# Kernel optimization log

Hardware: AMD Instinct MI355X
Metric: run time of the kernel (lower is better)

## Reference

```python
import jax, jax.numpy as jnp
import numpy as np

F = 256          # number of features (input_size)
H1, H2, H3 = 128, 64, 32
OUT = 1          # output_size


def setup_inputs() -> dict:
    key = jax.random.key(0)
    ks = jax.random.split(key, 10)
    B = 8192
    # Kaiming-uniform-ish small init; exact init doesn't matter for a math reference.
    def w(k, shape, fan_in):
        lim = 1.0 / np.sqrt(fan_in)
        return jax.random.uniform(k, shape, jnp.float32, -lim, lim)
    return {
        "x": jax.random.normal(ks[0], (B, F), dtype=jnp.float32),
        "W1": w(ks[1], (F, H1), 1),          # Linear(1 -> H1) per feature
        "b1": w(ks[2], (F, H1), 1),
        "W2": w(ks[3], (F, H1, H2), H1),
        "b2": w(ks[4], (F, H2), H1),
        "W3": w(ks[5], (F, H2, H3), H2),
        "b3": w(ks[6], (F, H3), H2),
        "W4": w(ks[7], (F, H3, OUT), H3),
        "b4": w(ks[8], (F, OUT), H3),
        "bias": jnp.zeros((OUT,), dtype=jnp.float32),
    }


def reference(x, W1, b1, W2, b2, W3, b3, W4, b4, bias):
    # Fused form of the per-feature FeatureNN loop (eval mode: dropout = identity).
    # Layer 1: scalar input per feature -> H1
    h = jax.nn.relu(x[:, :, None] * W1[None, :, :] + b1[None, :, :])   # [B,F,H1]
    h = jax.nn.relu(jnp.einsum('bfh,fhk->bfk', h, W2) + b2[None])      # [B,F,H2]
    h = jax.nn.relu(jnp.einsum('bfh,fhk->bfk', h, W3) + b3[None])      # [B,F,H3]
    f_out = jnp.einsum('bfh,fhk->bfk', h, W4) + b4[None]               # [B,F,OUT]
    # torch.cat(dim=1).sum(dim=1, keepdim=True): sum over features and output cols
    out = jnp.sum(f_out, axis=(1, 2), keepdims=False)[:, None] + bias[None, :]
    return out  # [B, OUT] with OUT==1
```

## Files before the change

kernel.cpp:

```cpp
#include <hip/hip_runtime.h>
#include <math.h>


#define NF   256
#define NH1  128
#define NH2  64
#define NH3  32
#define NB   8192

#define NRANK 129
#define ROW4  17
#define ROWH  136

typedef float    f32x4 __attribute__((ext_vector_type(4)));
typedef unsigned u32x4 __attribute__((ext_vector_type(4)));
typedef _Float16 h16x2 __attribute__((ext_vector_type(2)));
typedef _Float16 h16x8 __attribute__((ext_vector_type(8)));

__device__ __forceinline__ unsigned pkh2(unsigned sw, unsigned sb, h16x2 xh) {
    h16x2 r = __builtin_elementwise_fma(xh, __builtin_bit_cast(h16x2, sw),
                                            __builtin_bit_cast(h16x2, sb));
    h16x2 hz = {(_Float16)0.f, (_Float16)0.f};
    return __builtin_bit_cast(unsigned, __builtin_elementwise_max(r, hz));
}

__global__ __launch_bounds__(256) void init_out_kernel(float* __restrict__ out,
                                                       const float* __restrict__ bias) {
    int i = blockIdx.x * 256 + threadIdx.x;
    if (i < NB) out[i] = bias[0];
}

__global__ __launch_bounds__(1024, 8) void nam_fused(
    const float* __restrict__ x,
    const float* __restrict__ W1, const float* __restrict__ b1,
    const float* __restrict__ W2, const float* __restrict__ b2,
    const float* __restrict__ W3, const float* __restrict__ b3,
    const float* __restrict__ W4, const float* __restrict__ b4,
    float* __restrict__ out)
{
    __shared__ u32x4 SP4[NRANK * ROW4];
    __shared__ float tkey[NH1];
    __shared__ int   tidx[NH1];
    __shared__ float w1s[NH1], b1s[NH1];
    __shared__ float Pbw[8][NH2], Pbb[8][NH2], Pdw[8][NH2], Pdb[8][NH2];

    const int f    = blockIdx.x >> 1;
    const int half = blockIdx.x & 1;
    const int t = (int)threadIdx.x;
    _Float16* SPh = (_Float16*)SP4;

    const float* __restrict__ gw2 = W2 + (size_t)f * NH1 * NH2;
    if (t < NH1) {
        float w  = W1[f * NH1 + t];
        float bb = b1[f * NH1 + t];
        w1s[t] = w; b1s[t] = bb;
        tkey[t] = (w != 0.0f) ? (-bb / w) : INFINITY;
        tidx[t] = t;
    }
    __syncthreads();

    for (int size = 2; size <= NH1; size <<= 1) {
        for (int stride = size >> 1; stride > 0; stride >>= 1) {
            if (t < 64) {
                int pos = ((t / stride) * (stride << 1)) + (t % stride);
                int par = pos + stride;
                bool up = ((pos & size) == 0);
                float a = tkey[pos], c = tkey[par];
                int  ia = tidx[pos], ic = tidx[par];
                if ((a > c) == up) {
                    tkey[pos] = c; tkey[par] = a;
                    tidx[pos] = ic; tidx[par] = ia;
                }
            }
            __syncthreads();
        }
    }

    if (t < 512) {
        const int k = t & 63, c = t >> 6;
        float bw = 0.0f, bbp = 0.0f, dw = 0.0f, db = 0.0f;
        #pragma unroll 4
        for (int i = 0; i < 16; ++i) {
            int j = c * 16 + i;
            float w = w1s[j], bv = b1s[j], w2v = gw2[j * NH2 + k];
            if (w < 0.0f) { bw = fmaf(w, w2v, bw); bbp = fmaf(bv, w2v, bbp); }
            else if (w == 0.0f && bv > 0.0f) { bbp = fmaf(bv, w2v, bbp); }
            int jj = tidx[c * 16 + i];
            float ww = w1s[jj], bv2 = b1s[jj], w2x = gw2[jj * NH2 + k];
            float s = (ww > 0.0f) ? 1.0f : ((ww < 0.0f) ? -1.0f : 0.0f);
            dw = fmaf(s * ww,  w2x, dw);
            db = fmaf(s * bv2, w2x, db);
        }
        Pbw[c][k] = bw; Pbb[c][k] = bbp; Pdw[c][k] = dw; Pdb[c][k] = db;
    }
    __syncthreads();
    if (t < 512) {
        const int k = t & 63, c = t >> 6;
        float accw = 0.0f;
        float accb = b2[f * NH2 + k];
        #pragma unroll
        for (int c2 = 0; c2 < 8; ++c2) { accw += Pbw[c2][k]; accb += Pbb[c2][k]; }
        for (int c2 = 0; c2 < c; ++c2) { accw += Pdw[c2][k]; accb += Pdb[c2][k]; }
        if (c == 0) {
            SPh[k]      = (_Float16)accw;
            SPh[64 + k] = (_Float16)accb;
        }
        #pragma unroll 4
        for (int i = 0; i < 16; ++i) {
            int r = c * 16 + i;
            int j = tidx[r];
            float w = w1s[j], bv = b1s[j], w2v = gw2[j * NH2 + k];
            float s = (w > 0.0f) ? 1.0f : ((w < 0.0f) ? -1.0f : 0.0f);
            accw = fmaf(s * w,  w2v, accw);
            accb = fmaf(s * bv, w2v, accb);
            SPh[(r + 1) * ROWH + k]      = (_Float16)accw;
            SPh[(r + 1) * ROWH + 64 + k] = (_Float16)accb;
        }
    }
    __syncthreads();

    const int lane = t & 63, wv = t >> 6;
    const int n = lane & 15, q = lane >> 4;

    const float* __restrict__ w3g = W3 + f * NH2 * NH3;
    h16x8 aT0lo, aT0hi, aT1lo, aT1hi;
    #pragma unroll
    for (int j = 0; j < 8; ++j) {
        int k = q * 8 + j;
        aT0lo[j] = (_Float16)w3g[k * NH3 + n];
        aT0hi[j] = (_Float16)w3g[(k + 32) * NH3 + n];
        aT1lo[j] = (_Float16)w3g[k * NH3 + n + 16];
        aT1hi[j] = (_Float16)w3g[(k + 32) * NH3 + n + 16];
    }
    float b3c[4], b3ch[4], w4c[4], w4ch[4];
    #pragma unroll
    for (int i = 0; i < 4; ++i) {
        b3c[i]  = b3[f * NH3 + q * 4 + i];
        b3ch[i] = b3[f * NH3 + 16 + q * 4 + i];
        w4c[i]  = W4[f * NH3 + q * 4 + i];
        w4ch[i] = W4[f * NH3 + 16 + q * 4 + i];
    }
    const float b4f = b4[f];

    #pragma unroll 1
    for (int round = 0; round < 16; ++round) {
        const int base = half * 4096 + (round * 16 + wv) * 16;
        const int b = base + n;
        const float xv = x[(size_t)b * NF + f];

        int r = 0;
        #pragma unroll
        for (int s = 64; s > 0; s >>= 1)
            if (tkey[r + s - 1] < xv) r += s;

        const int ro = r * ROW4;
        u32x4 SW0 = SP4[ro + q],     SW1 = SP4[ro + 4 + q];
        u32x4 SB0 = SP4[ro + 8 + q], SB1 = SP4[ro + 12 + q];

        const h16x2 xh = {(_Float16)xv, (_Float16)xv};
        u32x4 d0, d1;
        d0.x = pkh2(SW0.x, SB0.x, xh);
        d0.y = pkh2(SW0.y, SB0.y, xh);
        d0.z = pkh2(SW0.z, SB0.z, xh);
        d0.w = pkh2(SW0.w, SB0.w, xh);
        d1.x = pkh2(SW1.x, SB1.x, xh);
        d1.y = pkh2(SW1.y, SB1.y, xh);
        d1.z = pkh2(SW1.z, SB1.z, xh);
        d1.w = pkh2(SW1.w, SB1.w, xh);
        h16x8 bf0 = __builtin_bit_cast(h16x8, d0);
        h16x8 bf1 = __builtin_bit_cast(h16x8, d1);

        f32x4 acc0 = {b3c[0], b3c[1], b3c[2], b3c[3]};
        f32x4 acc1 = {b3ch[0], b3ch[1], b3ch[2], b3ch[3]};
        acc0 = __builtin_amdgcn_mfma_f32_16x16x32_f16(aT0lo, bf0, acc0, 0, 0, 0);
        acc0 = __builtin_amdgcn_mfma_f32_16x16x32_f16(aT0hi, bf1, acc0, 0, 0, 0);
        acc1 = __builtin_amdgcn_mfma_f32_16x16x32_f16(aT1lo, bf0, acc1, 0, 0, 0);
        acc1 = __builtin_amdgcn_mfma_f32_16x16x32_f16(aT1hi, bf1, acc1, 0, 0, 0);

        float p = fmaxf(acc0[0], 0.0f) * w4c[0] + fmaxf(acc1[0], 0.0f) * w4ch[0]
                + fmaxf(acc0[1], 0.0f) * w4c[1] + fmaxf(acc1[1], 0.0f) * w4ch[1]
                + fmaxf(acc0[2], 0.0f) * w4c[2] + fmaxf(acc1[2], 0.0f) * w4ch[2]
                + fmaxf(acc0[3], 0.0f) * w4c[3] + fmaxf(acc1[3], 0.0f) * w4ch[3];
        p += __shfl_xor(p, 16);
        p += __shfl_xor(p, 32);
        if (lane < 16) atomicAdd(&out[base + lane], p + b4f);
    }
}

extern "C" void kernel_launch(void* const* d_in, const int* in_sizes, int n_in,
                              void* d_out, int out_size, void* d_ws, size_t ws_size,
                              hipStream_t stream) {
    const float* x    = (const float*)d_in[0];
    const float* W1   = (const float*)d_in[1];
    const float* b1   = (const float*)d_in[2];
    const float* W2   = (const float*)d_in[3];
    const float* b2   = (const float*)d_in[4];
    const float* W3   = (const float*)d_in[5];
    const float* b3   = (const float*)d_in[6];
    const float* W4   = (const float*)d_in[7];
    const float* b4   = (const float*)d_in[8];
    const float* bias = (const float*)d_in[9];
    float* out = (float*)d_out;

    init_out_kernel<<<NB / 256, 256, 0, stream>>>(out, bias);
    nam_fused<<<NF * 2, 1024, 0, stream>>>(x, W1, b1, W2, b2,
                                           W3, b3, W4, b4, out);
}
```

Before: 126.4 us.

## Switch layer-3 MFMA to 32x32x16 tiles and hoist top binary-search levels to registers

Each wave now processes 32 batch rows per round with four 32x32x16 f16 MFMAs instead of 16 rows with four 16x16x32 MFMAs, halving the number of rounds, per-row shuffle reductions and atomic-issue rounds. The first three levels of the breakpoint binary search are resolved from tkey values cached in registers, which removes three shared-memory loads per lookup. In exchange each thread holds more accumulator and weight registers, which may pressure occupancy under the 1024x8 launch bounds.

```diff
diff --git a/kernel.cpp b/kernel.cpp
--- a/kernel.cpp
+++ b/kernel.cpp
@@ -12,10 +12,10 @@
 #define ROW4  17
 #define ROWH  136
 
-typedef float    f32x4 __attribute__((ext_vector_type(4)));
-typedef unsigned u32x4 __attribute__((ext_vector_type(4)));
-typedef _Float16 h16x2 __attribute__((ext_vector_type(2)));
-typedef _Float16 h16x8 __attribute__((ext_vector_type(8)));
+typedef float    f32x16 __attribute__((ext_vector_type(16)));
+typedef unsigned u32x4  __attribute__((ext_vector_type(4)));
+typedef _Float16 h16x2  __attribute__((ext_vector_type(2)));
+typedef _Float16 h16x8  __attribute__((ext_vector_type(8)));
 
 __device__ __forceinline__ unsigned pkh2(unsigned sw, unsigned sb, h16x2 xh) {
     h16x2 r = __builtin_elementwise_fma(xh, __builtin_bit_cast(h16x2, sw),
@@ -120,70 +120,82 @@
     __syncthreads();
 
     const int lane = t & 63, wv = t >> 6;
-    const int n = lane & 15, q = lane >> 4;
+    const int n = lane & 31, q2 = lane >> 5;
 
     const float* __restrict__ w3g = W3 + f * NH2 * NH3;
-    h16x8 aT0lo, aT0hi, aT1lo, aT1hi;
+    h16x8 A0, A1, A2, A3;
     #pragma unroll
     for (int j = 0; j < 8; ++j) {
-        int k = q * 8 + j;
-        aT0lo[j] = (_Float16)w3g[k * NH3 + n];
-        aT0hi[j] = (_Float16)w3g[(k + 32) * NH3 + n];
-        aT1lo[j] = (_Float16)w3g[k * NH3 + n + 16];
-        aT1hi[j] = (_Float16)w3g[(k + 32) * NH3 + n + 16];
-    }
-    float b3c[4], b3ch[4], w4c[4], w4ch[4];
+        int kk = q2 * 8 + j;
+        A0[j] = (_Float16)w3g[kk * NH3 + n];
+        A1[j] = (_Float16)w3g[(kk + 16) * NH3 + n];
+        A2[j] = (_Float16)w3g[(kk + 32) * NH3 + n];
+        A3[j] = (_Float16)w3g[(kk + 48) * NH3 + n];
+    }
+    float b3r[16], w4r[16];
     #pragma unroll
-    for (int i = 0; i < 4; ++i) {
-        b3c[i]  = b3[f * NH3 + q * 4 + i];
-        b3ch[i] = b3[f * NH3 + 16 + q * 4 + i];
-        w4c[i]  = W4[f * NH3 + q * 4 + i];
-        w4ch[i] = W4[f * NH3 + 16 + q * 4 + i];
+    for (int reg = 0; reg < 16; ++reg) {
+        int row = (reg & 3) + 8 * (reg >> 2) + 4 * q2;
+        b3r[reg] = b3[f * NH3 + row];
+        w4r[reg] = W4[f * NH3 + row];
     }
     const float b4f = b4[f];
+    const float t63 = tkey[63], t31 = tkey[31], t95 = tkey[95];
+    const float t15 = tkey[15], t47 = tkey[47], t79 = tkey[79], t111 = tkey[111];
 
     #pragma unroll 1
-    for (int round = 0; round < 16; ++round) {
-        const int base = half * 4096 + (round * 16 + wv) * 16;
-        const int b = base + n;
-        const float xv = x[(size_t)b * NF + f];
-
-        int r = 0;
-        #pragma unroll
-        for (int s = 64; s > 0; s >>= 1)
+    for (int round = 0; round < 8; ++round) {
+        const int base = half * 4096 + (round * 16 + wv) * 32;
+        const float xv = x[(size_t)(base + n) * NF + f];
+
+        int r = (t63 < xv) ? 64 : 0;
+        {
+            float l1 = (r & 64) ? t95 : t31;
+            if (l1 < xv) r += 32;
+            float m0 = (r & 64) ? t79  : t15;
+            float m1 = (r & 64) ? t111 : t47;
+            float l2 = (r & 32) ? m1 : m0;
+            if (l2 < xv) r += 16;
+        }
+        #pragma unroll
+        for (int s = 8; s > 0; s >>= 1)
             if (tkey[r + s - 1] < xv) r += s;
 
         const int ro = r * ROW4;
-        u32x4 SW0 = SP4[ro + q],     SW1 = SP4[ro + 4 + q];
-        u32x4 SB0 = SP4[ro + 8 + q], SB1 = SP4[ro + 12 + q];
+        u32x4 SW0 = SP4[ro + q2],      SW1 = SP4[ro + 2 + q2];
+        u32x4 SW2 = SP4[ro + 4 + q2],  SW3 = SP4[ro + 6 + q2];
+        u32x4 SB0 = SP4[ro + 8 + q2],  SB1 = SP4[ro + 10 + q2];
+        u32x4 SB2 = SP4[ro + 12 + q2], SB3 = SP4[ro + 14 + q2];
 
         const h16x2 xh = {(_Float16)xv, (_Float16)xv};
-        u32x4 d0, d1;
-        d0.x = pkh2(SW0.x, SB0.x, xh);
-        d0.y = pkh2(SW0.y, SB0.y, xh);
-        d0.z = pkh2(SW0.z, SB0.z, xh);
-        d0.w = pkh2(SW0.w, SB0.w, xh);
-        d1.x = pkh2(SW1.x, SB1.x, xh);
-        d1.y = pkh2(SW1.y, SB1.y, xh);
-        d1.z = pkh2(SW1.z, SB1.z, xh);
-        d1.w = pkh2(SW1.w, SB1.w, xh);
-        h16x8 bf0 = __builtin_bit_cast(h16x8, d0);
-        h16x8 bf1 = __builtin_bit_cast(h16x8, d1);
-
-        f32x4 acc0 = {b3c[0], b3c[1], b3c[2], b3c[3]};
-        f32x4 acc1 = {b3ch[0], b3ch[1], b3ch[2], b3ch[3]};
-        acc0 = __builtin_amdgcn_mfma_f32_16x16x32_f16(aT0lo, bf0, acc0, 0, 0, 0);
-        acc0 = __builtin_amdgcn_mfma_f32_16x16x32_f16(aT0hi, bf1, acc0, 0, 0, 0);
-        acc1 = __builtin_amdgcn_mfma_f32_16x16x32_f16(aT1lo, bf0, acc1, 0, 0, 0);
-        acc1 = __builtin_amdgcn_mfma_f32_16x16x32_f16(aT1hi, bf1, acc1, 0, 0, 0);
-
-        float p = fmaxf(acc0[0], 0.0f) * w4c[0] + fmaxf(acc1[0], 0.0f) * w4ch[0]
-                + fmaxf(acc0[1], 0.0f) * w4c[1] + fmaxf(acc1[1], 0.0f) * w4ch[1]
-                + fmaxf(acc0[2], 0.0f) * w4c[2] + fmaxf(acc1[2], 0.0f) * w4ch[2]
-                + fmaxf(acc0[3], 0.0f) * w4c[3] + fmaxf(acc1[3], 0.0f) * w4ch[3];
-        p += __shfl_xor(p, 16);
+        u32x4 d0, d1, d2, d3;
+        d0.x = pkh2(SW0.x, SB0.x, xh); d0.y = pkh2(SW0.y, SB0.y, xh);
+        d0.z = pkh2(SW0.z, SB0.z, xh); d0.w = pkh2(SW0.w, SB0.w, xh);
+        d1.x = pkh2(SW1.x, SB1.x, xh); d1.y = pkh2(SW1.y, SB1.y, xh);
+        d1.z = pkh2(SW1.z, SB1.z, xh); d1.w = pkh2(SW1.w, SB1.w, xh);
+        d2.x = pkh2(SW2.x, SB2.x, xh); d2.y = pkh2(SW2.y, SB2.y, xh);
+        d2.z = pkh2(SW2.z, SB2.z, xh); d2.w = pkh2(SW2.w, SB2.w, xh);
+        d3.x = pkh2(SW3.x, SB3.x, xh); d3.y = pkh2(SW3.y, SB3.y, xh);
+        d3.z = pkh2(SW3.z, SB3.z, xh); d3.w = pkh2(SW3.w, SB3.w, xh);
+        h16x8 B0 = __builtin_bit_cast(h16x8, d0);
+        h16x8 B1 = __builtin_bit_cast(h16x8, d1);
+        h16x8 B2 = __builtin_bit_cast(h16x8, d2);
+        h16x8 B3 = __builtin_bit_cast(h16x8, d3);
+
+        f32x16 acc;
+        #pragma unroll
+        for (int reg = 0; reg < 16; ++reg) acc[reg] = b3r[reg];
+        acc = __builtin_amdgcn_mfma_f32_32x32x16_f16(A0, B0, acc, 0, 0, 0);
+        acc = __builtin_amdgcn_mfma_f32_32x32x16_f16(A1, B1, acc, 0, 0, 0);
+        acc = __builtin_amdgcn_mfma_f32_32x32x16_f16(A2, B2, acc, 0, 0, 0);
+        acc = __builtin_amdgcn_mfma_f32_32x32x16_f16(A3, B3, acc, 0, 0, 0);
+
+        float p = 0.0f;
+        #pragma unroll
+        for (int reg = 0; reg < 16; ++reg)
+            p = fmaf(fmaxf(acc[reg], 0.0f), w4r[reg], p);
         p += __shfl_xor(p, 32);
-        if (lane < 16) atomicAdd(&out[base + lane], p + b4f);
+        if (lane < 32) atomicAdd(&out[base + lane], p + b4f);
     }
 }
 
```

After: 225.5 us. 1.78x slower.
